# Optimization experiments

Hardware: AMD Instinct MI355X
Metric: run time of the kernel (lower is better)

## Reference

```python
import jax, jax.numpy as jnp
import numpy as np

B, C, H, Wd = 16, 512, 56, 56
WCH = 128  # W_ch: projection rank of phi/rou


def setup_inputs() -> dict:
    key = jax.random.key(0)
    ks = jax.random.split(key, 8)
    s = 0.02
    return {
        "x": jax.random.normal(ks[0], (B, C, H, Wd), dtype=jnp.float32),
        "y": jax.random.normal(ks[1], (B, C, H, Wd), dtype=jnp.float32),
        # phi: Conv2d(C, WCH, 1) -> weight [WCH, C], bias [WCH]
        "phi_w": jax.random.normal(ks[2], (WCH, C), dtype=jnp.float32) * s,
        "phi_b": jnp.zeros((WCH,), dtype=jnp.float32),
        # rou: Conv2d(C, WCH, 1) applied to globally pooled y -> acts as Linear
        "rou_w": jax.random.normal(ks[3], (WCH, C), dtype=jnp.float32) * s,
        "rou_b": jnp.zeros((WCH,), dtype=jnp.float32),
        # zeta: Linear(C, C)
        "zeta_w": jax.random.normal(ks[4], (C, C), dtype=jnp.float32) * s,
        "zeta_b": jnp.zeros((C,), dtype=jnp.float32),
    }


def reference(x, y, phi_w, phi_b, rou_w, rou_b, zeta_w, zeta_b):
    b, c, h, w = x.shape
    hw = h * w
    # phi_xT = relu(phi(x)).view(B, WCH, HW); phi_x = transpose -> [B, HW, WCH]
    phi_xT = jax.nn.relu(jnp.einsum('kc,bchw->bkhw', phi_w, x) + phi_b[None, :, None, None])
    phi_x = phi_xT.reshape(b, -1, hw).transpose(0, 2, 1)  # [B, HW, WCH]
    # rou_y = sigmoid(rou(global_avg_pool(y))) -> [B, WCH]
    pooled = y.mean(axis=(2, 3))  # [B, C]
    rou_y = jax.nn.sigmoid(pooled @ rou_w.T + rou_b)  # [B, WCH]
    # D_i = sum_j (phi_x diag(rou) phi_x^T)_{ij} = sum_k phi_x[i,k] rou[k] s[k]
    s = phi_x.sum(axis=1)  # [B, WCH], column sums
    D = jnp.einsum('bnk,bk,bk->bn', phi_x, rou_y, s)  # [B, HW]
    inv_sqrt = 1.0 / jnp.sqrt(D + 1e-8)
    P = phi_x * inv_sqrt[..., None]  # diag(D^-1/2) @ phi_x, [B, HW, WCH]
    # x.view(B, -1, C): raw row-major reshape of [B,C,H,W] (NOT a transpose)
    x_trans = x.reshape(b, hw, c)
    # LX = x_trans - P diag(rou) P^T x_trans, re-associated right-to-left
    t = jnp.einsum('bnk,bnc->bkc', P, x_trans)          # P^T x_trans, [B, WCH, C]
    LX = x_trans - jnp.einsum('bnk,bk,bkc->bnc', P, rou_y, t)
    # zeta Linear + dropout(eval: identity) + relu, residual add
    out = jax.nn.relu(LX @ zeta_w.T + zeta_b)
    return x + out.reshape(b, c, h, w)
```

## Files before the change

### kernel.cpp

```cpp
#include <hip/hip_runtime.h>
#include <math.h>

#define B_  16
#define C_  512
#define HW_ 3136
#define K_  128
#define CHW (C_ * HW_)

typedef __bf16 bf16x8_t __attribute__((ext_vector_type(8)));
typedef __bf16 bf16x4_t __attribute__((ext_vector_type(4)));
typedef float floatx4  __attribute__((ext_vector_type(4)));

typedef const __attribute__((address_space(1))) void* gas_ptr;
typedef __attribute__((address_space(3))) void*       las_ptr;

static __device__ __forceinline__ unsigned short bfbits(__bf16 v) {
    return __builtin_bit_cast(unsigned short, v);
}

__device__ __forceinline__ void stage128x64(const __bf16* __restrict__ base, long ld,
                                            int row0, int rowmax, int k0,
                                            __bf16* lds, int t) {
    int w = t >> 6;
    #pragma unroll
    for (int i = 0; i < 4; ++i) {
        int u = i * 256 + t;
        int m = u >> 3, slot = u & 7;
        int kg = slot ^ (m & 7);
        int r = row0 + m; if (r > rowmax) r = rowmax;
        const __bf16* g = base + (long)r * ld + (k0 + kg * 8);
        __bf16* l = lds + (size_t)(i * 256 + w * 64) * 8;
        __builtin_amdgcn_global_load_lds((gas_ptr)g, (las_ptr)l, 16, 0, 0);
    }
}

__device__ __forceinline__ void stage_tsum(const float* __restrict__ tp, int p0,
                                           char* lds, int t) {
    const long BKC = (long)B_ * K_ * C_;
    #pragma unroll
    for (int i = 0; i < 4; ++i) {
        int u = i * 256 + t;
        int m = u >> 3, slot = u & 7;
        int kg = slot ^ (m & 7);
        const float* g = tp + (long)m * C_ + (p0 + kg * 8);
        float4 a0 = *reinterpret_cast<const float4*>(g);
        float4 a1 = *reinterpret_cast<const float4*>(g + 4);
        #pragma unroll
        for (int p = 1; p < 7; ++p) {
            const float* gp = g + (long)p * BKC;
            float4 v0 = *reinterpret_cast<const float4*>(gp);
            float4 v1 = *reinterpret_cast<const float4*>(gp + 4);
            a0.x += v0.x; a0.y += v0.y; a0.z += v0.z; a0.w += v0.w;
            a1.x += v1.x; a1.y += v1.y; a1.z += v1.z; a1.w += v1.w;
        }
        bf16x8_t pk;
        pk[0] = (__bf16)a0.x; pk[1] = (__bf16)a0.y; pk[2] = (__bf16)a0.z; pk[3] = (__bf16)a0.w;
        pk[4] = (__bf16)a1.x; pk[5] = (__bf16)a1.y; pk[6] = (__bf16)a1.z; pk[7] = (__bf16)a1.w;
        *reinterpret_cast<bf16x8_t*>(lds + (size_t)u * 16) = pk;
    }
}

__device__ __forceinline__ void stage_tr(const __bf16* __restrict__ src, long ld,
                                         int r0, int p0, char* Bs, int t) {
    int rg = t & 15;
    int pp2 = (t >> 4) * 2;
    #pragma unroll
    for (int ci = 0; ci < 2; ++ci) {
        int cc = pp2 + ci * 32;
        const __bf16* g0 = src + (long)(p0 + cc) * ld + r0 + rg * 8;
        bf16x8_t v0 = *(const bf16x8_t*)g0;
        bf16x8_t v1 = *(const bf16x8_t*)(g0 + ld);
        int r8 = cc >> 3, sub = (cc & 7) >> 1;
        #pragma unroll
        for (int j = 0; j < 8; ++j) {
            int row = rg * 8 + j;
            int slot = (r8 + row + (row >> 3)) & 7;
            unsigned int pr = ((unsigned int)bfbits(v1[j]) << 16) | bfbits(v0[j]);
            *(unsigned int*)(Bs + row * 144 + slot * 16 + sub * 4) = pr;
        }
    }
}

__device__ __forceinline__ void mma_step64(const char* As, const char* Bs,
                                           floatx4 acc[4][4], int aoff, int boff,
                                           int q, int lxor) {
    #pragma unroll
    for (int h = 0; h < 2; ++h) {
        int s = (((h * 4 + q) ^ lxor) << 4);
        bf16x8_t af[4], bf[4];
        #pragma unroll
        for (int i = 0; i < 4; ++i) af[i] = *(const bf16x8_t*)(As + aoff + i * 2048 + s);
        #pragma unroll
        for (int i = 0; i < 4; ++i) bf[i] = *(const bf16x8_t*)(Bs + boff + i * 2048 + s);
        #pragma unroll
        for (int mi = 0; mi < 4; ++mi)
            #pragma unroll
            for (int ni = 0; ni < 4; ++ni)
                acc[mi][ni] = __builtin_amdgcn_mfma_f32_16x16x32_bf16(af[mi], bf[ni], acc[mi][ni], 0, 0, 0);
    }
}

__device__ __forceinline__ void mma_step_mix(const char* As, const char* Bs,
                                             floatx4 acc[4][4], int lm, int q,
                                             int wrow, int wcol) {
    int lxor = lm & 7;
    int aoff = (wrow * 64 + lm) * 128;
    #pragma unroll
    for (int h = 0; h < 2; ++h) {
        int g = h * 4 + q;
        int sa = (g ^ lxor) << 4;
        bf16x8_t af[4], bf[4];
        #pragma unroll
        for (int i = 0; i < 4; ++i) af[i] = *(const bf16x8_t*)(As + aoff + i * 2048 + sa);
        #pragma unroll
        for (int i = 0; i < 4; ++i) {
            int brow = wcol * 64 + i * 16 + lm;
            int slot = (g + brow + (brow >> 3)) & 7;
            bf[i] = *(const bf16x8_t*)(Bs + brow * 144 + slot * 16);
        }
        #pragma unroll
        for (int mi = 0; mi < 4; ++mi)
            #pragma unroll
            for (int ni = 0; ni < 4; ++ni)
                acc[mi][ni] = __builtin_amdgcn_mfma_f32_16x16x32_bf16(af[mi], bf[ni], acc[mi][ni], 0, 0, 0);
    }
}

__device__ __forceinline__ void mma_step_rot2(const char* As, const char* Bs,
                                              floatx4 acc[4][4], int lm, int q,
                                              int wrow, int wcol) {
    #pragma unroll
    for (int h = 0; h < 2; ++h) {
        int g = h * 4 + q;
        bf16x8_t af[4], bf[4];
        #pragma unroll
        for (int i = 0; i < 4; ++i) {
            int arow = wrow * 64 + i * 16 + lm;
            int aslot = (g + arow + (arow >> 3)) & 7;
            af[i] = *(const bf16x8_t*)(As + arow * 144 + aslot * 16);
        }
        #pragma unroll
        for (int i = 0; i < 4; ++i) {
            int brow = wcol * 64 + i * 16 + lm;
            int bslot = (g + brow + (brow >> 3)) & 7;
            bf[i] = *(const bf16x8_t*)(Bs + brow * 144 + bslot * 16);
        }
        #pragma unroll
        for (int mi = 0; mi < 4; ++mi)
            #pragma unroll
            for (int ni = 0; ni < 4; ++ni)
                acc[mi][ni] = __builtin_amdgcn_mfma_f32_16x16x32_bf16(af[mi], bf[ni], acc[mi][ni], 0, 0, 0);
    }
}

__global__ __launch_bounds__(256) void k_prep(const float* __restrict__ x,
                                              const float* __restrict__ y,
                                              const float* __restrict__ phi_w,
                                              const float* __restrict__ zeta_w,
                                              __bf16* __restrict__ xbf2,
                                              float* __restrict__ pooled,
                                              __bf16* __restrict__ pwbf,
                                              __bf16* __restrict__ zwbf,
                                              float* __restrict__ sbuf) {
    int gid = blockIdx.x;
    int t = threadIdx.x;
    if (gid < 12704) {
        const float* src; __bf16* dst; long off;
        if (gid < 32)       { src = phi_w;  dst = pwbf; off = (long)gid * 2048; }
        else if (gid < 160) { src = zeta_w; dst = zwbf; off = (long)(gid - 32) * 2048; }
        else                { src = x;      dst = xbf2; off = (long)(gid - 160) * 2048; }
        long i = off + (long)t * 8;
        float4 v0 = *reinterpret_cast<const float4*>(src + i);
        float4 v1 = *reinterpret_cast<const float4*>(src + i + 4);
        bf16x8_t r;
        r[0] = (__bf16)v0.x; r[1] = (__bf16)v0.y; r[2] = (__bf16)v0.z; r[3] = (__bf16)v0.w;
        r[4] = (__bf16)v1.x; r[5] = (__bf16)v1.y; r[6] = (__bf16)v1.z; r[7] = (__bf16)v1.w;
        *reinterpret_cast<bf16x8_t*>(dst + i) = r;
    } else if (gid < 20896) {
        int bc = gid - 12704;
        const float* yp = y + (long)bc * HW_;
        float acc = 0.f;
        #pragma unroll
        for (int i = 0; i < 4; ++i) {
            int n4 = t + i * 256;
            if (n4 < 784) {
                float4 v = *reinterpret_cast<const float4*>(yp + (long)n4 * 4);
                acc += v.x + v.y + v.z + v.w;
            }
        }
        #pragma unroll
        for (int off = 32; off > 0; off >>= 1) acc += __shfl_xor(acc, off, 64);
        __shared__ float red[4];
        if ((t & 63) == 0) red[t >> 6] = acc;
        __syncthreads();
        if (t == 0) pooled[bc] = (red[0] + red[1] + red[2] + red[3]) * (1.0f / HW_);
    } else {
        for (int i = t; i < B_ * K_; i += 256) sbuf[i] = 0.f;
    }
}


__global__ __launch_bounds__(256) void k_phi_m(const __bf16* __restrict__ xbf2,
                                               const __bf16* __restrict__ pwbf,
                                               const float* __restrict__ phi_b,
                                               const float* __restrict__ pooled,
                                               const float* __restrict__ rou_w,
                                               const float* __restrict__ rou_b,
                                               float* __restrict__ rou_y,
                                               __bf16* __restrict__ phi_nk,
                                               float* __restrict__ sbuf) {
    int b = blockIdx.y;
    int n0 = blockIdx.x * 128;
    __shared__ __attribute__((aligned(16))) char smem[2 * 34816];
    int t = threadIdx.x, w = t >> 6, lane = t & 63;
    int lm = lane & 15, q = lane >> 4;
    int wrow = w >> 1, wcol = w & 1;

    if (blockIdx.x == 0) {
        int k = t >> 1, h = t & 1;
        const float* pr = pooled + b * C_ + h * 256;
        const float* wr = rou_w + (long)k * C_ + h * 256;
        float a = 0.f;
        #pragma unroll 4
        for (int c = 0; c < 256; c += 4) {
            float4 w4 = *reinterpret_cast<const float4*>(wr + c);
            float4 p4 = *reinterpret_cast<const float4*>(pr + c);
            a += w4.x * p4.x + w4.y * p4.y + w4.z * p4.z + w4.w * p4.w;
        }
        a += __shfl_xor(a, 1, 64);
        if (h == 0) rou_y[b * K_ + k] = 1.0f / (1.0f + expf(-(a + rou_b[k])));
    }

    floatx4 acc[4][4];
    #pragma unroll
    for (int i = 0; i < 4; ++i)
        #pragma unroll
        for (int j = 0; j < 4; ++j) acc[i][j] = (floatx4){0.f, 0.f, 0.f, 0.f};

    const __bf16* Bb = xbf2 + (long)b * CHW;

    stage128x64(pwbf, C_, 0, K_ - 1, 0, (__bf16*)smem, t);
    stage_tr(Bb, HW_, n0, 0, smem + 16384, t);
    __syncthreads();
    int cur = 0;
    #pragma unroll
    for (int s = 0; s < 8; ++s) {
        char* cb = smem + cur * 34816;
        if (s < 7) {
            char* nb = smem + (cur ^ 1) * 34816;
            int p0 = (s + 1) * 64;
            stage128x64(pwbf, C_, 0, K_ - 1, p0, (__bf16*)nb, t);
            stage_tr(Bb, HW_, n0, p0, nb + 16384, t);
        }
        mma_step_mix(cb, cb + 16384, acc, lm, q, wrow, wcol);
        __syncthreads();
        cur ^= 1;
    }
    #pragma unroll
    for (int mi = 0; mi < 4; ++mi) {
        int kb = wrow * 64 + mi * 16 + q * 4;
        float4 pb = *reinterpret_cast<const float4*>(phi_b + kb);
        float pbv[4] = {pb.x, pb.y, pb.z, pb.w};
        float sv[4] = {0.f, 0.f, 0.f, 0.f};
        #pragma unroll
        for (int ni = 0; ni < 4; ++ni) {
            int n = n0 + wcol * 64 + ni * 16 + lm;
            if (n < HW_) {
                bf16x4_t pack;
                #pragma unroll
                for (int r = 0; r < 4; ++r) {
                    float v = fmaxf(acc[mi][ni][r] + pbv[r], 0.f);
                    pack[r] = (__bf16)v;
                    sv[r] += v;
                }
                *reinterpret_cast<bf16x4_t*>(phi_nk + ((long)b * HW_ + n) * K_ + kb) = pack;
            }
        }
        #pragma unroll
        for (int r = 0; r < 4; ++r) {
            float v = sv[r];
            v += __shfl_xor(v, 1, 64); v += __shfl_xor(v, 2, 64);
            v += __shfl_xor(v, 4, 64); v += __shfl_xor(v, 8, 64);
            if (lm == 0) atomicAdd(&sbuf[b * K_ + kb + r], v);
        }
    }
}

__global__ __launch_bounds__(256) void k_d2(__bf16* __restrict__ phi_nk,
                                            const float* __restrict__ rou_y,
                                            const float* __restrict__ s,
                                            float* __restrict__ inv_s) {
    int b = blockIdx.y;
    __shared__ float ws[K_];
    int t = threadIdx.x;
    if (t < K_) ws[t] = rou_y[b * K_ + t] * s[b * K_ + t];
    __syncthreads();
    int w = t >> 6, lane = t & 63;
    int sub = lane >> 4, lm = lane & 15;
    int n = blockIdx.x * 16 + w * 4 + sub;
    __bf16* p = phi_nk + ((long)b * HW_ + n) * K_ + lm * 8;
    bf16x8_t v = *reinterpret_cast<bf16x8_t*>(p);
    float f[8];
    #pragma unroll
    for (int j = 0; j < 8; ++j) f[j] = (float)v[j];
    float d = 0.f;
    #pragma unroll
    for (int j = 0; j < 8; ++j) d += f[j] * ws[lm * 8 + j];
    d += __shfl_xor(d, 1, 64); d += __shfl_xor(d, 2, 64);
    d += __shfl_xor(d, 4, 64); d += __shfl_xor(d, 8, 64);
    float inv = rsqrtf(d + 1e-8f);
    bf16x8_t o;
    #pragma unroll
    for (int j = 0; j < 8; ++j) o[j] = (__bf16)(f[j] * inv);
    *reinterpret_cast<bf16x8_t*>(p) = o;
    if (lm == 0) inv_s[b * HW_ + n] = inv;
}

__global__ __launch_bounds__(256) void k_t_m(const __bf16* __restrict__ pnk,
                                             const __bf16* __restrict__ xbf2,
                                             float* __restrict__ t_part) {
    int gid = blockIdx.x;
    int rlo = gid & 7, cc4 = (gid >> 3) & 3, r8 = gid >> 5;
    int r = r8 * 8 + rlo;
    int b = r / 7, nch = r % 7;
    int c0 = cc4 * 128;
    __shared__ __attribute__((aligned(16))) char smem[2 * 36864];
    int t = threadIdx.x, w = t >> 6, lane = t & 63;
    int lm = lane & 15, q = lane >> 4;
    int wrow = w >> 1, wcol = w & 1;
    floatx4 acc[4][4];
    #pragma unroll
    for (int i = 0; i < 4; ++i)
        #pragma unroll
        for (int j = 0; j < 4; ++j) acc[i][j] = (floatx4){0.f, 0.f, 0.f, 0.f};

    const __bf16* Ab = pnk + (long)b * (long)HW_ * K_;
    const __bf16* Bb = xbf2 + (long)b * CHW;

    int pstart = nch * 448;
    stage_tr(Ab, K_, 0, pstart, smem, t);
    stage_tr(Bb, C_, c0, pstart, smem + 18432, t);
    __syncthreads();
    int cur = 0;
    #pragma unroll
    for (int s = 0; s < 7; ++s) {
        char* cb = smem + cur * 36864;
        if (s < 6) {
            char* nb = smem + (cur ^ 1) * 36864;
            int p0 = pstart + (s + 1) * 64;
            stage_tr(Ab, K_, 0, p0, nb, t);
            stage_tr(Bb, C_, c0, p0, nb + 18432, t);
        }
        mma_step_rot2(cb, cb + 18432, acc, lm, q, wrow, wcol);
        __syncthreads();
        cur ^= 1;
    }
    float* outp = t_part + ((long)nch * B_ + b) * K_ * C_;
    #pragma unroll
    for (int mi = 0; mi < 4; ++mi) {
        int kb = wrow * 64 + mi * 16 + q * 4;
        #pragma unroll
        for (int ni = 0; ni < 4; ++ni) {
            int c = c0 + wcol * 64 + ni * 16 + lm;
            #pragma unroll
            for (int rr = 0; rr < 4; ++rr)
                outp[(long)(kb + rr) * C_ + c] = acc[mi][ni][rr];
        }
    }
}

__global__ __launch_bounds__(256) void k_tz_m(const __bf16* __restrict__ zwbf,
                                              const float* __restrict__ t_part,
                                              const float* __restrict__ rou_y,
                                              __bf16* __restrict__ tzT) {
    int b = blockIdx.y;
    int c0 = blockIdx.x * 128;
    __shared__ __attribute__((aligned(16))) char smem[2 * 32768];
    int t = threadIdx.x, w = t >> 6, lane = t & 63;
    int lm = lane & 15, q = lane >> 4;
    int wrow = w >> 1, wcol = w & 1;
    floatx4 acc[4][4];
    #pragma unroll
    for (int i = 0; i < 4; ++i)
        #pragma unroll
        for (int j = 0; j < 4; ++j) acc[i][j] = (floatx4){0.f, 0.f, 0.f, 0.f};

    const float* Tb = t_part + (long)b * K_ * C_;
    int lxor = lm & 7;
    int aoff = (wrow * 64 + lm) * 128;
    int boff = (wcol * 64 + lm) * 128;

    stage128x64(zwbf, C_, c0, C_ - 1, 0, (__bf16*)smem, t);
    stage_tsum(Tb, 0, smem + 16384, t);
    __syncthreads();
    int cur = 0;
    #pragma unroll
    for (int s = 0; s < 8; ++s) {
        char* cb = smem + cur * 32768;
        if (s < 7) {
            char* nb = smem + (cur ^ 1) * 32768;
            int p0 = (s + 1) * 64;
            stage128x64(zwbf, C_, c0, C_ - 1, p0, (__bf16*)nb, t);
            stage_tsum(Tb, p0, nb + 16384, t);
        }
        mma_step64(cb, cb + 16384, acc, aoff, boff, q, lxor);
        __syncthreads();
        cur ^= 1;
    }
    #pragma unroll
    for (int mi = 0; mi < 4; ++mi) {
        int c = c0 + wrow * 64 + mi * 16 + q * 4;
        #pragma unroll
        for (int ni = 0; ni < 4; ++ni) {
            int k = wcol * 64 + ni * 16 + lm;
            float rk = rou_y[b * K_ + k];
            #pragma unroll
            for (int rr = 0; rr < 4; ++rr)
                tzT[((long)b * C_ + c + rr) * K_ + k] = (__bf16)(-rk * acc[mi][ni][rr]);
        }
    }
}

__global__ __launch_bounds__(256) void k_out_m(const __bf16* __restrict__ xbf2,
                                               const __bf16* __restrict__ zwbf,
                                               const __bf16* __restrict__ pnk,
                                               const __bf16* __restrict__ tzT,
                                               const float* __restrict__ zeta_b,
                                               float* __restrict__ out) {
    int gid = blockIdx.x;
    int rlo = gid & 7, cc4 = (gid >> 3) & 3, r8 = gid >> 5;
    int r = r8 * 8 + rlo;
    int b = r / 25, nt = r % 25;
    int n0 = nt * 128;
    int c0 = cc4 * 128;
    __shared__ __attribute__((aligned(16))) char smem[2 * 32768];
    int t = threadIdx.x, w = t >> 6, lane = t & 63;
    int lm = lane & 15, q = lane >> 4;
    int wrow = w >> 1, wcol = w & 1;
    floatx4 acc[4][4];
    #pragma unroll
    for (int i = 0; i < 4; ++i)
        #pragma unroll
        for (int j = 0; j < 4; ++j) acc[i][j] = (floatx4){0.f, 0.f, 0.f, 0.f};

    int lxor = lm & 7;
    int aoff = (wrow * 64 + lm) * 128;
    int boff = (wcol * 64 + lm) * 128;

    const __bf16* A1 = xbf2 + (long)b * CHW;
    const __bf16* A2 = pnk + (long)b * (long)HW_ * K_;
    const __bf16* B2 = tzT + (long)b * (long)C_ * K_;

    stage128x64(A1,   C_, n0, HW_ - 1, 0, (__bf16*)smem, t);
    stage128x64(zwbf, C_, c0, C_ - 1, 0, (__bf16*)(smem + 16384), t);
    __syncthreads();
    int cur = 0;
    #pragma unroll
    for (int s = 0; s < 10; ++s) {
        char* cb = smem + cur * 32768;
        if (s < 9) {
            char* nb = smem + (cur ^ 1) * 32768;
            int sn = s + 1;
            if (sn < 8) {
                int p0 = sn * 64;
                stage128x64(A1,   C_, n0, HW_ - 1, p0, (__bf16*)nb, t);
                stage128x64(zwbf, C_, c0, C_ - 1, p0, (__bf16*)(nb + 16384), t);
            } else {
                int p0 = (sn - 8) * 64;
                stage128x64(A2, K_, n0, HW_ - 1, p0, (__bf16*)nb, t);
                stage128x64(B2, K_, c0, C_ - 1, p0, (__bf16*)(nb + 16384), t);
            }
        }
        mma_step64(cb, cb + 16384, acc, aoff, boff, q, lxor);
        __syncthreads();
        cur ^= 1;
    }
    float* ep = (float*)smem;
    const __bf16* xres = xbf2 + (long)b * CHW;
    int lr = t >> 3, lc = (t & 7) * 16;
    #pragma unroll
    for (int ch = 0; ch < 4; ++ch) {
        __syncthreads();
        if (wrow == (ch >> 1)) {
            #pragma unroll
            for (int mm = 0; mm < 2; ++mm) {
                int mi = (ch & 1) * 2 + mm;
                #pragma unroll
                for (int ni = 0; ni < 4; ++ni)
                    #pragma unroll
                    for (int rr = 0; rr < 4; ++rr)
                        ep[(mm * 16 + q * 4 + rr) * 132 + wcol * 64 + ni * 16 + lm] = acc[mi][ni][rr];
            }
        }
        __syncthreads();
        int n = n0 + ch * 32 + lr;
        if (n < HW_) {
            long rowbase = (long)n * C_ + c0 + lc;
            bf16x8_t x0 = *(const bf16x8_t*)(xres + rowbase);
            bf16x8_t x1 = *(const bf16x8_t*)(xres + rowbase + 8);
            float xv[16];
            #pragma unroll
            for (int j = 0; j < 8; ++j) { xv[j] = (float)x0[j]; xv[8 + j] = (float)x1[j]; }
            float* orow = out + (long)b * CHW + rowbase;
            #pragma unroll
            for (int jj = 0; jj < 4; ++jj) {
                float4 zb = *reinterpret_cast<const float4*>(zeta_b + c0 + lc + jj * 4);
                float4 e  = *reinterpret_cast<const float4*>(&ep[lr * 132 + lc + jj * 4]);
                float4 o;
                o.x = xv[jj * 4 + 0] + fmaxf(e.x + zb.x, 0.f);
                o.y = xv[jj * 4 + 1] + fmaxf(e.y + zb.y, 0.f);
                o.z = xv[jj * 4 + 2] + fmaxf(e.z + zb.z, 0.f);
                o.w = xv[jj * 4 + 3] + fmaxf(e.w + zb.w, 0.f);
                *reinterpret_cast<float4*>(orow + jj * 4) = o;
            }
        }
    }
}

extern "C" void kernel_launch(void* const* d_in, const int* in_sizes, int n_in,
                              void* d_out, int out_size, void* d_ws, size_t ws_size,
                              hipStream_t stream) {
    const float* x      = (const float*)d_in[0];
    const float* y      = (const float*)d_in[1];
    const float* phi_w  = (const float*)d_in[2];
    const float* phi_b  = (const float*)d_in[3];
    const float* rou_w  = (const float*)d_in[4];
    const float* rou_b  = (const float*)d_in[5];
    const float* zeta_w = (const float*)d_in[6];
    const float* zeta_b = (const float*)d_in[7];
    float* out = (float*)d_out;

    char* p = (char*)d_ws;
    __bf16* xbf2   = (__bf16*)p; p += (size_t)B_ * CHW * 2;
    __bf16* phi_nk = (__bf16*)p; p += (size_t)B_ * K_ * HW_ * 2;
    float*  t_part = (float*) p; p += (size_t)7 * B_ * K_ * C_ * 4;
    __bf16* tzT    = (__bf16*)p; p += (size_t)B_ * C_ * K_ * 2;
    __bf16* pwbf   = (__bf16*)p; p += (size_t)K_ * C_ * 2;
    __bf16* zwbf   = (__bf16*)p; p += (size_t)C_ * C_ * 2;
    float*  pooled = (float*) p; p += (size_t)B_ * C_ * 4;
    float*  rou_y  = (float*) p; p += (size_t)B_ * K_ * 4;
    float*  sbuf   = (float*) p; p += (size_t)B_ * K_ * 4;
    float*  inv_s  = (float*) p; p += (size_t)B_ * HW_ * 4;

    k_prep <<<20897, 256, 0, stream>>>(x, y, phi_w, zeta_w, xbf2, pooled, pwbf, zwbf, sbuf);
    k_phi_m<<<dim3(25, B_), 256, 0, stream>>>(xbf2, pwbf, phi_b, pooled, rou_w, rou_b,
                                              rou_y, phi_nk, sbuf);
    k_d2   <<<dim3(HW_ / 16, B_), 256, 0, stream>>>(phi_nk, rou_y, sbuf, inv_s);
    k_t_m  <<<448, 256, 0, stream>>>(phi_nk, xbf2, t_part);
    k_tz_m <<<dim3(C_ / 128, B_), 256, 0, stream>>>(zwbf, t_part, rou_y, tzT);
    k_out_m<<<1600, 256, 0, stream>>>(xbf2, zwbf, phi_nk, tzT, zeta_b, out);
}
```

Baseline: 402.2 us.

## Split partial-sum reduction into its own kernel and use grid-stride prep blocks

```diff
diff --git a/kernel.cpp b/kernel.cpp
--- a/kernel.cpp
+++ b/kernel.cpp
@@ -6,6 +6,9 @@
 #define HW_ 3136
 #define K_  128
 #define CHW (C_ * HW_)
+
+#define NCAST 1232
+#define NPOOL 812
 
 typedef __bf16 bf16x8_t __attribute__((ext_vector_type(8)));
 typedef __bf16 bf16x4_t __attribute__((ext_vector_type(4)));
@@ -31,32 +34,6 @@
         const __bf16* g = base + (long)r * ld + (k0 + kg * 8);
         __bf16* l = lds + (size_t)(i * 256 + w * 64) * 8;
         __builtin_amdgcn_global_load_lds((gas_ptr)g, (las_ptr)l, 16, 0, 0);
-    }
-}
-
-__device__ __forceinline__ void stage_tsum(const float* __restrict__ tp, int p0,
-                                           char* lds, int t) {
-    const long BKC = (long)B_ * K_ * C_;
-    #pragma unroll
-    for (int i = 0; i < 4; ++i) {
-        int u = i * 256 + t;
-        int m = u >> 3, slot = u & 7;
-        int kg = slot ^ (m & 7);
-        const float* g = tp + (long)m * C_ + (p0 + kg * 8);
-        float4 a0 = *reinterpret_cast<const float4*>(g);
-        float4 a1 = *reinterpret_cast<const float4*>(g + 4);
-        #pragma unroll
-        for (int p = 1; p < 7; ++p) {
-            const float* gp = g + (long)p * BKC;
-            float4 v0 = *reinterpret_cast<const float4*>(gp);
-            float4 v1 = *reinterpret_cast<const float4*>(gp + 4);
-            a0.x += v0.x; a0.y += v0.y; a0.z += v0.z; a0.w += v0.w;
-            a1.x += v1.x; a1.y += v1.y; a1.z += v1.z; a1.w += v1.w;
-        }
-        bf16x8_t pk;
-        pk[0] = (__bf16)a0.x; pk[1] = (__bf16)a0.y; pk[2] = (__bf16)a0.z; pk[3] = (__bf16)a0.w;
-        pk[4] = (__bf16)a1.x; pk[5] = (__bf16)a1.y; pk[6] = (__bf16)a1.z; pk[7] = (__bf16)a1.w;
-        *reinterpret_cast<bf16x8_t*>(lds + (size_t)u * 16) = pk;
     }
 }
 
@@ -164,36 +141,40 @@
                                               float* __restrict__ sbuf) {
     int gid = blockIdx.x;
     int t = threadIdx.x;
-    if (gid < 12704) {
-        const float* src; __bf16* dst; long off;
-        if (gid < 32)       { src = phi_w;  dst = pwbf; off = (long)gid * 2048; }
-        else if (gid < 160) { src = zeta_w; dst = zwbf; off = (long)(gid - 32) * 2048; }
-        else                { src = x;      dst = xbf2; off = (long)(gid - 160) * 2048; }
-        long i = off + (long)t * 8;
-        float4 v0 = *reinterpret_cast<const float4*>(src + i);
-        float4 v1 = *reinterpret_cast<const float4*>(src + i + 4);
-        bf16x8_t r;
-        r[0] = (__bf16)v0.x; r[1] = (__bf16)v0.y; r[2] = (__bf16)v0.z; r[3] = (__bf16)v0.w;
-        r[4] = (__bf16)v1.x; r[5] = (__bf16)v1.y; r[6] = (__bf16)v1.z; r[7] = (__bf16)v1.w;
-        *reinterpret_cast<bf16x8_t*>(dst + i) = r;
-    } else if (gid < 20896) {
-        int bc = gid - 12704;
-        const float* yp = y + (long)bc * HW_;
-        float acc = 0.f;
-        #pragma unroll
-        for (int i = 0; i < 4; ++i) {
-            int n4 = t + i * 256;
-            if (n4 < 784) {
-                float4 v = *reinterpret_cast<const float4*>(yp + (long)n4 * 4);
-                acc += v.x + v.y + v.z + v.w;
+    if (gid < NCAST) {
+        for (int chunk = gid; chunk < 12704; chunk += NCAST) {
+            const float* src; __bf16* dst; long off;
+            if (chunk < 32)       { src = phi_w;  dst = pwbf; off = (long)chunk * 2048; }
+            else if (chunk < 160) { src = zeta_w; dst = zwbf; off = (long)(chunk - 32) * 2048; }
+            else                  { src = x;      dst = xbf2; off = (long)(chunk - 160) * 2048; }
+            long i = off + (long)t * 8;
+            float4 v0 = *reinterpret_cast<const float4*>(src + i);
+            float4 v1 = *reinterpret_cast<const float4*>(src + i + 4);
+            bf16x8_t r;
+            r[0] = (__bf16)v0.x; r[1] = (__bf16)v0.y; r[2] = (__bf16)v0.z; r[3] = (__bf16)v0.w;
+            r[4] = (__bf16)v1.x; r[5] = (__bf16)v1.y; r[6] = (__bf16)v1.z; r[7] = (__bf16)v1.w;
+            *reinterpret_cast<bf16x8_t*>(dst + i) = r;
+        }
+    } else if (gid < NCAST + NPOOL) {
+        __shared__ float red[4];
+        for (int bc = gid - NCAST; bc < B_ * C_; bc += NPOOL) {
+            const float* yp = y + (long)bc * HW_;
+            float acc = 0.f;
+            #pragma unroll
+            for (int i = 0; i < 4; ++i) {
+                int n4 = t + i * 256;
+                if (n4 < 784) {
+                    float4 v = *reinterpret_cast<const float4*>(yp + (long)n4 * 4);
+                    acc += v.x + v.y + v.z + v.w;
+                }
             }
-        }
-        #pragma unroll
-        for (int off = 32; off > 0; off >>= 1) acc += __shfl_xor(acc, off, 64);
-        __shared__ float red[4];
-        if ((t & 63) == 0) red[t >> 6] = acc;
-        __syncthreads();
-        if (t == 0) pooled[bc] = (red[0] + red[1] + red[2] + red[3]) * (1.0f / HW_);
+            #pragma unroll
+            for (int off = 32; off > 0; off >>= 1) acc += __shfl_xor(acc, off, 64);
+            if ((t & 63) == 0) red[t >> 6] = acc;
+            __syncthreads();
+            if (t == 0) pooled[bc] = (red[0] + red[1] + red[2] + red[3]) * (1.0f / HW_);
+            __syncthreads();
+        }
     } else {
         for (int i = t; i < B_ * K_; i += 256) sbuf[i] = 0.f;
     }
@@ -369,8 +350,23 @@
     }
 }
 
+__global__ __launch_bounds__(256) void k_tred(const float* __restrict__ t_part,
+                                              __bf16* __restrict__ t_bf) {
+    const long BKC = (long)B_ * K_ * C_;
+    long i = ((long)blockIdx.x * 256 + threadIdx.x) * 4;
+    float4 s = *reinterpret_cast<const float4*>(t_part + i);
+    #pragma unroll
+    for (int p = 1; p < 7; ++p) {
+        float4 v = *reinterpret_cast<const float4*>(t_part + p * BKC + i);
+        s.x += v.x; s.y += v.y; s.z += v.z; s.w += v.w;
+    }
+    bf16x4_t o;
+    o[0] = (__bf16)s.x; o[1] = (__bf16)s.y; o[2] = (__bf16)s.z; o[3] = (__bf16)s.w;
+    *reinterpret_cast<bf16x4_t*>(t_bf + i) = o;
+}
+
 __global__ __launch_bounds__(256) void k_tz_m(const __bf16* __restrict__ zwbf,
-                                              const float* __restrict__ t_part,
+                                              const __bf16* __restrict__ t_bf,
                                               const float* __restrict__ rou_y,
                                               __bf16* __restrict__ tzT) {
     int b = blockIdx.y;
@@ -385,13 +381,13 @@
         #pragma unroll
         for (int j = 0; j < 4; ++j) acc[i][j] = (floatx4){0.f, 0.f, 0.f, 0.f};
 
-    const float* Tb = t_part + (long)b * K_ * C_;
+    const __bf16* Bb = t_bf + (long)b * K_ * C_;
     int lxor = lm & 7;
     int aoff = (wrow * 64 + lm) * 128;
     int boff = (wcol * 64 + lm) * 128;
 
     stage128x64(zwbf, C_, c0, C_ - 1, 0, (__bf16*)smem, t);
-    stage_tsum(Tb, 0, smem + 16384, t);
+    stage128x64(Bb,   C_, 0, K_ - 1, 0, (__bf16*)(smem + 16384), t);
     __syncthreads();
     int cur = 0;
     #pragma unroll
@@ -401,7 +397,7 @@
             char* nb = smem + (cur ^ 1) * 32768;
             int p0 = (s + 1) * 64;
             stage128x64(zwbf, C_, c0, C_ - 1, p0, (__bf16*)nb, t);
-            stage_tsum(Tb, p0, nb + 16384, t);
+            stage128x64(Bb,   C_, 0, K_ - 1, p0, (__bf16*)(nb + 16384), t);
         }
         mma_step64(cb, cb + 16384, acc, aoff, boff, q, lxor);
         __syncthreads();
@@ -534,6 +530,7 @@
     __bf16* xbf2   = (__bf16*)p; p += (size_t)B_ * CHW * 2;
     __bf16* phi_nk = (__bf16*)p; p += (size_t)B_ * K_ * HW_ * 2;
     float*  t_part = (float*) p; p += (size_t)7 * B_ * K_ * C_ * 4;
+    __bf16* t_bf   = (__bf16*)p; p += (size_t)B_ * K_ * C_ * 2;
     __bf16* tzT    = (__bf16*)p; p += (size_t)B_ * C_ * K_ * 2;
     __bf16* pwbf   = (__bf16*)p; p += (size_t)K_ * C_ * 2;
     __bf16* zwbf   = (__bf16*)p; p += (size_t)C_ * C_ * 2;
@@ -542,11 +539,13 @@
     float*  sbuf   = (float*) p; p += (size_t)B_ * K_ * 4;
     float*  inv_s  = (float*) p; p += (size_t)B_ * HW_ * 4;
 
-    k_prep <<<20897, 256, 0, stream>>>(x, y, phi_w, zeta_w, xbf2, pooled, pwbf, zwbf, sbuf);
+    k_prep <<<NCAST + NPOOL + 1, 256, 0, stream>>>(x, y, phi_w, zeta_w, xbf2, pooled,
+                                                   pwbf, zwbf, sbuf);
     k_phi_m<<<dim3(25, B_), 256, 0, stream>>>(xbf2, pwbf, phi_b, pooled, rou_w, rou_b,
                                               rou_y, phi_nk, sbuf);
     k_d2   <<<dim3(HW_ / 16, B_), 256, 0, stream>>>(phi_nk, rou_y, sbuf, inv_s);
     k_t_m  <<<448, 256, 0, stream>>>(phi_nk, xbf2, t_part);
-    k_tz_m <<<dim3(C_ / 128, B_), 256, 0, stream>>>(zwbf, t_part, rou_y, tzT);
+    k_tred <<<(B_ * K_ * C_) / 1024, 256, 0, stream>>>(t_part, t_bf);
+    k_tz_m <<<dim3(C_ / 128, B_), 256, 0, stream>>>(zwbf, t_bf, rou_y, tzT);
     k_out_m<<<1600, 256, 0, stream>>>(xbf2, zwbf, phi_nk, tzT, zeta_b, out);
 }
```

Measured after the change: 389.3 us. 1.03x faster.
